# Performance work log

Measured on AMD Instinct MI355X. Metric: run time of the kernel, lower is better.

## Reference

```python
import jax, jax.numpy as jnp
import numpy as np

LMAX = 8
RES_BETA = 32   # Gauss-Legendre points in beta (>= 2*LMAX+1 -> exact quadrature for product)
RES_ALPHA = 63  # uniform points in alpha (>= 2*(2*LMAX)+1)
BATCH = 16384
DIM = (LMAX + 1) ** 2  # 81 real SH coefficients, flat index i = l*l + l + m


def _normalized_assoc_legendre(lmax, y):
    # P[b, l, m] = orthonormalized associated Legendre \bar{P}_l^m(y), 0<=m<=l,
    # normalized so that int_{-1}^{1} Pbar_l^m Pbar_l'^m dy = delta_{ll'} / (2*pi).
    n = len(y)
    P = np.zeros((n, lmax + 1, lmax + 1))
    sx = np.sqrt(np.clip(1.0 - y * y, 0.0, None))
    P[:, 0, 0] = np.sqrt(1.0 / (4.0 * np.pi))
    for m in range(1, lmax + 1):
        P[:, m, m] = -np.sqrt((2.0 * m + 1.0) / (2.0 * m)) * sx * P[:, m - 1, m - 1]
    for m in range(lmax):
        P[:, m + 1, m] = np.sqrt(2.0 * m + 3.0) * y * P[:, m, m]
    for m in range(lmax + 1):
        for l in range(m + 2, lmax + 1):
            a = np.sqrt((4.0 * l * l - 1.0) / (l * l - m * m))
            b = np.sqrt(((l - 1.0) ** 2 - m * m) / (4.0 * (l - 1.0) ** 2 - 1.0))
            P[:, l, m] = a * (y * P[:, l - 1, m] - b * P[:, l - 2, m])
    return P


def _s2grid_basis():
    # Gauss-Legendre nodes y=cos(beta) and weights (integrate sin(beta) d(beta) exactly)
    y, w = np.polynomial.legendre.leggauss(RES_BETA)
    P = _normalized_assoc_legendre(LMAX, y)
    alphas = 2.0 * np.pi * np.arange(RES_ALPHA) / RES_ALPHA
    shb = np.zeros((RES_BETA, DIM))   # Legendre part, per flat (l,m) index
    sha = np.zeros((RES_ALPHA, DIM))  # Fourier part, per flat (l,m) index
    s2 = np.sqrt(2.0)
    for l in range(LMAX + 1):
        for m in range(-l, l + 1):
            i = l * l + l + m
            shb[:, i] = P[:, l, abs(m)]
            if m == 0:
                sha[:, i] = 1.0
            elif m > 0:
                sha[:, i] = s2 * np.cos(m * alphas)
            else:
                sha[:, i] = s2 * np.sin(-m * alphas)
    qw = w * (2.0 * np.pi / RES_ALPHA)  # combined beta quadrature + alpha trapezoid weight
    return (shb.astype(np.float32), sha.astype(np.float32), qw.astype(np.float32))


def setup_inputs() -> dict:
    key = jax.random.key(0)
    k1, k2 = jax.random.split(key)
    shb, sha, qw = _s2grid_basis()
    return {
        "input1": jax.random.normal(k1, (BATCH, DIM), dtype=jnp.float32),
        "input2": jax.random.normal(k2, (BATCH, DIM), dtype=jnp.float32),
        "shb": jnp.asarray(shb),
        "sha": jnp.asarray(sha),
        "qw": jnp.asarray(qw),
    }


def _to_s2grid(x, shb, sha):
    # x: [Z, D] -> grid: [Z, res_beta, res_alpha]
    t = jnp.einsum('zi,bi->zbi', x, shb)        # Legendre expansion along beta
    return jnp.einsum('zbi,ai->zba', t, sha)    # Fourier synthesis along alpha


def _from_s2grid(g, shb, sha, qw):
    # g: [Z, res_beta, res_alpha] -> coeffs: [Z, D]
    t = jnp.einsum('zba,ai->zbi', g, sha)       # Fourier analysis along alpha
    return jnp.einsum('zbi,bi,b->zi', t, shb, qw)  # Legendre projection with quadrature


def reference(input1, input2, shb, sha, qw):
    g1 = _to_s2grid(input1, shb, sha)
    g2 = _to_s2grid(input2, shb, sha)
    return _from_s2grid(g1 * g2, shb, sha, qw)
```

## Files before the change

### kernel.cpp

```cpp
#include <hip/hip_runtime.h>

#define DIM 81
#define RA  63
#define RB  32
#define ZT  32
#define XS  104
#define OS  100

#define OFF_SHAA 0
#define OFF_SHAT 12288
#define OFF_SHBH 24576
#define OFF_SHBQ 30720
#define WS_NEED  43008

typedef _Float16 half8 __attribute__((ext_vector_type(8)));
typedef __fp16  fp16x2 __attribute__((ext_vector_type(2)));
typedef float floatx16 __attribute__((ext_vector_type(16)));

union H8U { unsigned u[4]; half8 h; };
union H2U { fp16x2 h; unsigned u; };

__global__ __launch_bounds__(256) void precompute_fact(
    const float* __restrict__ shb, const float* __restrict__ sha,
    const float* __restrict__ qw, char* __restrict__ wsp)
{
    _Float16* shaAP = (_Float16*)(wsp + OFF_SHAA);
    _Float16* shaTP = (_Float16*)(wsp + OFF_SHAT);
    _Float16* shbHP = (_Float16*)(wsp + OFF_SHBH);
    float*    shbqP = (float*)(wsp + OFF_SHBQ);

    int idx = blockIdx.x * 256 + threadIdx.x;
    if (idx < 6144) {
        int j = idx & 7, lane = (idx >> 3) & 63, g = idx >> 9;
        int at = g / 6, kk = g - at * 6;
        int a = at * 32 + (lane & 31);
        int i = kk * 16 + (lane >> 5) * 8 + j;
        float v = (a < RA && i < DIM) ? sha[a * DIM + i] : 0.f;
        shaAP[idx] = (_Float16)v;
    } else if (idx < 12288) {
        int t = idx - 6144;
        int j = t & 7, lane = (t >> 3) & 63, g = t >> 9;
        int it = g >> 2, ks = g & 3;
        int a = ks * 16 + (lane >> 5) * 8 + j;
        int i = it * 32 + (lane & 31);
        float v = (a < RA && i < DIM) ? sha[a * DIM + i] : 0.f;
        shaTP[t] = (_Float16)v;
    } else if (idx < 15360) {
        int t = idx - 12288;
        int j = t & 7, hi = (t >> 3) & 1, g = t >> 4;
        int b = g / 6, kk = g - b * 6;
        int i = kk * 16 + hi * 8 + j;
        float v = (i < DIM) ? shb[b * DIM + i] : 0.f;
        shbHP[t] = (_Float16)v;
    } else if (idx < 18432) {
        int t = idx - 15360;
        int l = t & 31, g = t >> 5;
        int b = g / 3, it = g - b * 3;
        int i = it * 32 + l;
        float v = (i < DIM) ? shb[b * DIM + i] * qw[b] : 0.f;
        shbqP[t] = v;
    }
}

__global__ __launch_bounds__(256, 1) void gaunt_fact(
    const float* __restrict__ x1, const float* __restrict__ x2,
    const char* __restrict__ wsp, float* __restrict__ out)
{
    const _Float16* shaAP = (const _Float16*)(wsp + OFF_SHAA);
    const _Float16* shaTP = (const _Float16*)(wsp + OFF_SHAT);
    const _Float16* shbHP = (const _Float16*)(wsp + OFF_SHBH);
    const float*    shbqP = (const float*)(wsp + OFF_SHBQ);

    __shared__ __align__(16) char lds[2 * ZT * OS * 4];
    _Float16* xp = (_Float16*)lds;
    float*    ob = (float*)lds;

    const int tid = threadIdx.x;
    const int z0  = blockIdx.x * ZT;

    #pragma unroll
    for (int in = 0; in < 2; ++in) {
        const float* src = in ? x2 : x1;
        _Float16* dst = xp + in * (ZT * XS);
        for (int idx = tid; idx < ZT * 96; idx += 256) {
            int r = idx / 96, c = idx - r * 96;
            float v = (c < DIM) ? src[(size_t)(z0 + r) * DIM + c] : 0.f;
            dst[r * XS + c] = (_Float16)v;
        }
    }
    __syncthreads();

    const int l = tid & 63, l31 = l & 31, hi = l >> 5;
    const int nw = tid >> 6;

    half8 xfr[2][6];
    #pragma unroll
    for (int in = 0; in < 2; ++in)
        #pragma unroll
        for (int kk = 0; kk < 6; ++kk)
            xfr[in][kk] = *(const half8*)(xp + in * (ZT * XS) + l31 * XS + kk * 16 + hi * 8);
    __syncthreads();

    half8 aAc[2][6];
    #pragma unroll
    for (int at = 0; at < 2; ++at)
        #pragma unroll
        for (int kk = 0; kk < 6; ++kk)
            aAc[at][kk] = *(const half8*)(shaAP + ((at * 6 + kk) * 64 + l) * 8);

    floatx16 accO[3];
    #pragma unroll
    for (int it = 0; it < 3; ++it)
        #pragma unroll
        for (int r = 0; r < 16; ++r) accO[it][r] = 0.f;

    #pragma unroll 1
    for (int bi = 0; bi < 8; ++bi) {
        const int b = nw * 8 + bi;

        const float s0 = shbqP[(b * 3 + 0) * 32 + l31];
        const float s1 = shbqP[(b * 3 + 1) * 32 + l31];
        const float s2 = shbqP[(b * 3 + 2) * 32 + l31];

        unsigned f[2][8];
        #pragma unroll
        for (int at = 0; at < 2; ++at) {
            floatx16 g0, g1;
            #pragma unroll
            for (int r = 0; r < 16; ++r) { g0[r] = 0.f; g1[r] = 0.f; }
            #pragma unroll
            for (int kk = 0; kk < 6; ++kk) {
                const half8 sf = *(const half8*)(shbHP + ((b * 6 + kk) * 2 + hi) * 8);
                const half8 aS = aAc[at][kk] * sf;
                g0 = __builtin_amdgcn_mfma_f32_32x32x16_f16(aS, xfr[0][kk], g0, 0, 0, 0);
                g1 = __builtin_amdgcn_mfma_f32_32x32x16_f16(aS, xfr[1][kk], g1, 0, 0, 0);
            }
            unsigned q[8];
            #pragma unroll
            for (int j = 0; j < 8; ++j) {
                H2U t;
                t.h = __builtin_amdgcn_cvt_pkrtz(g0[2 * j] * g1[2 * j], g0[2 * j + 1] * g1[2 * j + 1]);
                q[j] = t.u;
            }
            asm volatile("v_permlane32_swap_b32 %0, %1" : "+v"(q[0]), "+v"(q[2]));
            asm volatile("v_permlane32_swap_b32 %0, %1" : "+v"(q[1]), "+v"(q[3]));
            asm volatile("v_permlane32_swap_b32 %0, %1" : "+v"(q[4]), "+v"(q[6]));
            asm volatile("v_permlane32_swap_b32 %0, %1" : "+v"(q[5]), "+v"(q[7]));
            #pragma unroll
            for (int w = 0; w < 8; ++w) f[at][w] = q[w];
        }

        #pragma unroll
        for (int it = 0; it < 3; ++it) {
            floatx16 R;
            #pragma unroll
            for (int r = 0; r < 16; ++r) R[r] = 0.f;
            #pragma unroll
            for (int at = 0; at < 2; ++at) {
                H8U a0, a1;
                a0.u[0] = f[at][0]; a0.u[1] = f[at][1]; a0.u[2] = f[at][2]; a0.u[3] = f[at][3];
                a1.u[0] = f[at][4]; a1.u[1] = f[at][5]; a1.u[2] = f[at][6]; a1.u[3] = f[at][7];
                half8 bT0 = *(const half8*)(shaTP + ((it * 4 + at * 2) * 64 + l) * 8);
                half8 bT1 = *(const half8*)(shaTP + ((it * 4 + at * 2 + 1) * 64 + l) * 8);
                R = __builtin_amdgcn_mfma_f32_32x32x16_f16(a0.h, bT0, R, 0, 0, 0);
                R = __builtin_amdgcn_mfma_f32_32x32x16_f16(a1.h, bT1, R, 0, 0, 0);
            }
            const float s = (it == 0) ? s0 : (it == 1) ? s1 : s2;
            accO[it] += R * s;
        }
    }

    if (nw >= 2) {
        float* buf = ob + (nw - 2) * (ZT * OS);
        #pragma unroll
        for (int it = 0; it < 3; ++it)
            #pragma unroll
            for (int r = 0; r < 16; ++r)
                buf[((r & 3) + 8 * (r >> 2) + 4 * hi) * OS + it * 32 + l31] = accO[it][r];
    }
    __syncthreads();
    if (nw < 2) {
        float* buf = ob + nw * (ZT * OS);
        #pragma unroll
        for (int it = 0; it < 3; ++it)
            #pragma unroll
            for (int r = 0; r < 16; ++r)
                accO[it][r] += buf[((r & 3) + 8 * (r >> 2) + 4 * hi) * OS + it * 32 + l31];
    }
    __syncthreads();
    if (nw < 2) {
        float* buf = ob + nw * (ZT * OS);
        #pragma unroll
        for (int it = 0; it < 3; ++it)
            #pragma unroll
            for (int r = 0; r < 16; ++r)
                buf[((r & 3) + 8 * (r >> 2) + 4 * hi) * OS + it * 32 + l31] = accO[it][r];
    }
    __syncthreads();

    for (int idx = tid; idx < ZT * DIM; idx += 256) {
        int zz = idx / DIM, ii = idx - zz * DIM;
        out[(size_t)z0 * DIM + idx] = ob[zz * OS + ii] + ob[ZT * OS + zz * OS + ii];
    }
}

__device__ __forceinline__ float wave_sum64(float v) {
    v += __int_as_float(__builtin_amdgcn_update_dpp(0, __float_as_int(v), 0x111, 0xf, 0xf, true));
    v += __int_as_float(__builtin_amdgcn_update_dpp(0, __float_as_int(v), 0x112, 0xf, 0xf, true));
    v += __int_as_float(__builtin_amdgcn_update_dpp(0, __float_as_int(v), 0x114, 0xf, 0xf, true));
    v += __int_as_float(__builtin_amdgcn_update_dpp(0, __float_as_int(v), 0x118, 0xf, 0xf, true));
    v += __int_as_float(__builtin_amdgcn_update_dpp(0, __float_as_int(v), 0x142, 0xf, 0xf, true));
    v += __int_as_float(__builtin_amdgcn_update_dpp(0, __float_as_int(v), 0x143, 0xf, 0xf, true));
    return v;
}

__global__ __launch_bounds__(256) void gaunt_s2grid_kernel(
    const float* __restrict__ x1, const float* __restrict__ x2,
    const float* __restrict__ shb, const float* __restrict__ sha,
    const float* __restrict__ qw, float* __restrict__ out)
{
    __shared__ float sha_s[64 * DIM];
    __shared__ float part[4 * DIM];
    const int tid = threadIdx.x;
    const int z = blockIdx.x;
    for (int idx = tid; idx < 64 * DIM; idx += 256)
        sha_s[idx] = (idx < RA * DIM) ? sha[idx] : 0.0f;
    __syncthreads();
    const int lane = tid & 63;
    const int w = __builtin_amdgcn_readfirstlane(tid >> 6);
    const int b0 = w * 8;
    const float* xz1 = x1 + (size_t)z * DIM;
    const float* xz2 = x2 + (size_t)z * DIM;
    const float* sha_row = sha_s + lane * DIM;
    float g1[8], g2[8];
    #pragma unroll
    for (int bb = 0; bb < 8; ++bb) { g1[bb] = 0.0f; g2[bb] = 0.0f; }
    #pragma unroll 4
    for (int i = 0; i < DIM; ++i) {
        const float sv = sha_row[i];
        const float t1 = xz1[i] * sv, t2 = xz2[i] * sv;
        #pragma unroll
        for (int bb = 0; bb < 8; ++bb) {
            const float h = shb[(b0 + bb) * DIM + i];
            g1[bb] = fmaf(h, t1, g1[bb]);
            g2[bb] = fmaf(h, t2, g2[bb]);
        }
    }
    float q[8];
    #pragma unroll
    for (int bb = 0; bb < 8; ++bb) q[bb] = g1[bb] * g2[bb] * qw[b0 + bb];
    #pragma unroll 4
    for (int i = 0; i < DIM; ++i) {
        float t = 0.0f;
        #pragma unroll
        for (int bb = 0; bb < 8; ++bb) t = fmaf(q[bb], shb[(b0 + bb) * DIM + i], t);
        float v = wave_sum64(t * sha_row[i]);
        if (lane == 63) part[w * DIM + i] = v;
    }
    __syncthreads();
    for (int i = tid; i < DIM; i += 256)
        out[(size_t)z * DIM + i] = part[i] + part[DIM + i] + part[2 * DIM + i] + part[3 * DIM + i];
}

extern "C" void kernel_launch(void* const* d_in, const int* in_sizes, int n_in,
                              void* d_out, int out_size, void* d_ws, size_t ws_size,
                              hipStream_t stream) {
    const float* x1  = (const float*)d_in[0];
    const float* x2  = (const float*)d_in[1];
    const float* shb = (const float*)d_in[2];
    const float* sha = (const float*)d_in[3];
    const float* qw  = (const float*)d_in[4];
    float* out = (float*)d_out;

    const int Z = in_sizes[0] / DIM;

    if (ws_size >= WS_NEED && (Z % ZT) == 0) {
        char* wsp = (char*)d_ws;
        precompute_fact<<<72, 256, 0, stream>>>(shb, sha, qw, wsp);
        gaunt_fact<<<Z / ZT, 256, 0, stream>>>(x1, x2, wsp, out);
    } else {
        gaunt_s2grid_kernel<<<Z, 256, 0, stream>>>(x1, x2, shb, sha, qw, out);
    }
}
```

Before: 42.83 us.

## Stage basis tables in LDS and software-pipeline the per-beta GEMM stages

Each block now copies the precomputed fp16/fp32 basis tables (about 43 KB) from global memory into shared memory and reads them from there instead of from global memory inside the loop. The beta loop is software-pipelined: the grid product for the next beta is computed before the analysis GEMM for the current one, so the two stages' MFMA and permlane work can interleave. The cost is more LDS per block (about 68 KB), which may limit co-resident blocks, a table copy in every block, and higher register pressure from holding two fragment sets.

```diff
diff --git a/kernel.cpp b/kernel.cpp
--- a/kernel.cpp
+++ b/kernel.cpp
@@ -11,7 +11,10 @@
 #define OFF_SHAT 12288
 #define OFF_SHBH 24576
 #define OFF_SHBQ 30720
-#define WS_NEED  43008
+#define TBL_BYTES 43008
+#define WS_NEED   43008
+#define L_XOB     43008
+#define LDS_BYTES (43008 + 25600)
 
 typedef _Float16 half8 __attribute__((ext_vector_type(8)));
 typedef __fp16  fp16x2 __attribute__((ext_vector_type(2)));
@@ -66,17 +69,20 @@
     const float* __restrict__ x1, const float* __restrict__ x2,
     const char* __restrict__ wsp, float* __restrict__ out)
 {
-    const _Float16* shaAP = (const _Float16*)(wsp + OFF_SHAA);
-    const _Float16* shaTP = (const _Float16*)(wsp + OFF_SHAT);
-    const _Float16* shbHP = (const _Float16*)(wsp + OFF_SHBH);
-    const float*    shbqP = (const float*)(wsp + OFF_SHBQ);
-
-    __shared__ __align__(16) char lds[2 * ZT * OS * 4];
-    _Float16* xp = (_Float16*)lds;
-    float*    ob = (float*)lds;
+    __shared__ __align__(16) char lds[LDS_BYTES];
+
+    const _Float16* shaA = (const _Float16*)(lds + OFF_SHAA);
+    const _Float16* shaT = (const _Float16*)(lds + OFF_SHAT);
+    const _Float16* shbH = (const _Float16*)(lds + OFF_SHBH);
+    const float*    shbq = (const float*)(lds + OFF_SHBQ);
+    _Float16* xp = (_Float16*)(lds + L_XOB);
+    float*    ob = (float*)(lds + L_XOB);
 
     const int tid = threadIdx.x;
     const int z0  = blockIdx.x * ZT;
+
+    for (int i = tid; i < TBL_BYTES / 16; i += 256)
+        ((uint4*)lds)[i] = ((const uint4*)wsp)[i];
 
     #pragma unroll
     for (int in = 0; in < 2; ++in) {
@@ -99,14 +105,14 @@
         #pragma unroll
         for (int kk = 0; kk < 6; ++kk)
             xfr[in][kk] = *(const half8*)(xp + in * (ZT * XS) + l31 * XS + kk * 16 + hi * 8);
-    __syncthreads();
 
     half8 aAc[2][6];
     #pragma unroll
     for (int at = 0; at < 2; ++at)
         #pragma unroll
         for (int kk = 0; kk < 6; ++kk)
-            aAc[at][kk] = *(const half8*)(shaAP + ((at * 6 + kk) * 64 + l) * 8);
+            aAc[at][kk] = *(const half8*)(shaA + ((at * 6 + kk) * 64 + l) * 8);
+    __syncthreads();
 
     floatx16 accO[3];
     #pragma unroll
@@ -114,15 +120,7 @@
         #pragma unroll
         for (int r = 0; r < 16; ++r) accO[it][r] = 0.f;
 
-    #pragma unroll 1
-    for (int bi = 0; bi < 8; ++bi) {
-        const int b = nw * 8 + bi;
-
-        const float s0 = shbqP[(b * 3 + 0) * 32 + l31];
-        const float s1 = shbqP[(b * 3 + 1) * 32 + l31];
-        const float s2 = shbqP[(b * 3 + 2) * 32 + l31];
-
-        unsigned f[2][8];
+    auto compute_f = [&](int b, unsigned fO[2][8]) {
         #pragma unroll
         for (int at = 0; at < 2; ++at) {
             floatx16 g0, g1;
@@ -130,7 +128,7 @@
             for (int r = 0; r < 16; ++r) { g0[r] = 0.f; g1[r] = 0.f; }
             #pragma unroll
             for (int kk = 0; kk < 6; ++kk) {
-                const half8 sf = *(const half8*)(shbHP + ((b * 6 + kk) * 2 + hi) * 8);
+                const half8 sf = *(const half8*)(shbH + ((b * 6 + kk) * 2 + hi) * 8);
                 const half8 aS = aAc[at][kk] * sf;
                 g0 = __builtin_amdgcn_mfma_f32_32x32x16_f16(aS, xfr[0][kk], g0, 0, 0, 0);
                 g1 = __builtin_amdgcn_mfma_f32_32x32x16_f16(aS, xfr[1][kk], g1, 0, 0, 0);
@@ -147,9 +145,14 @@
             asm volatile("v_permlane32_swap_b32 %0, %1" : "+v"(q[4]), "+v"(q[6]));
             asm volatile("v_permlane32_swap_b32 %0, %1" : "+v"(q[5]), "+v"(q[7]));
             #pragma unroll
-            for (int w = 0; w < 8; ++w) f[at][w] = q[w];
+            for (int w = 0; w < 8; ++w) fO[at][w] = q[w];
         }
-
+    };
+
+    auto gemm2_acc = [&](int b, const unsigned fI[2][8]) {
+        const float s0 = shbq[(b * 3 + 0) * 32 + l31];
+        const float s1 = shbq[(b * 3 + 1) * 32 + l31];
+        const float s2 = shbq[(b * 3 + 2) * 32 + l31];
         #pragma unroll
         for (int it = 0; it < 3; ++it) {
             floatx16 R;
@@ -158,17 +161,30 @@
             #pragma unroll
             for (int at = 0; at < 2; ++at) {
                 H8U a0, a1;
-                a0.u[0] = f[at][0]; a0.u[1] = f[at][1]; a0.u[2] = f[at][2]; a0.u[3] = f[at][3];
-                a1.u[0] = f[at][4]; a1.u[1] = f[at][5]; a1.u[2] = f[at][6]; a1.u[3] = f[at][7];
-                half8 bT0 = *(const half8*)(shaTP + ((it * 4 + at * 2) * 64 + l) * 8);
-                half8 bT1 = *(const half8*)(shaTP + ((it * 4 + at * 2 + 1) * 64 + l) * 8);
+                a0.u[0] = fI[at][0]; a0.u[1] = fI[at][1]; a0.u[2] = fI[at][2]; a0.u[3] = fI[at][3];
+                a1.u[0] = fI[at][4]; a1.u[1] = fI[at][5]; a1.u[2] = fI[at][6]; a1.u[3] = fI[at][7];
+                half8 bT0 = *(const half8*)(shaT + ((it * 4 + at * 2) * 64 + l) * 8);
+                half8 bT1 = *(const half8*)(shaT + ((it * 4 + at * 2 + 1) * 64 + l) * 8);
                 R = __builtin_amdgcn_mfma_f32_32x32x16_f16(a0.h, bT0, R, 0, 0, 0);
                 R = __builtin_amdgcn_mfma_f32_32x32x16_f16(a1.h, bT1, R, 0, 0, 0);
             }
             const float s = (it == 0) ? s0 : (it == 1) ? s1 : s2;
             accO[it] += R * s;
         }
-    }
+    };
+
+    unsigned fc[2][8], fn[2][8];
+    compute_f(nw * 8, fc);
+    #pragma unroll 1
+    for (int bi = 0; bi < 7; ++bi) {
+        compute_f(nw * 8 + bi + 1, fn);
+        gemm2_acc(nw * 8 + bi, fc);
+        #pragma unroll
+        for (int at = 0; at < 2; ++at)
+            #pragma unroll
+            for (int w = 0; w < 8; ++w) fc[at][w] = fn[at][w];
+    }
+    gemm2_acc(nw * 8 + 7, fc);
 
     if (nw >= 2) {
         float* buf = ob + (nw - 2) * (ZT * OS);
```

Measured after the change: 45.89 us. 1.07x slower.

## Software-pipeline beta loop, hoist shaT fragments to registers, vectorize input load

Applied to the files above, without the earlier changes.

The beta loop is software-pipelined so the forward GEMM and product for the next beta row are issued before the analysis GEMM of the current row, letting independent MFMA chains interleave. The shaT B-fragments are now loaded once into registers instead of being reloaded every iteration. The input staging uses float4 loads and packed half4 stores in place of scalar element copies. This adds register pressure from the extra f buffer and 12 cached half8 fragments, which could cause spills at one wave per SIMD.

```diff
diff --git a/kernel.cpp b/kernel.cpp
--- a/kernel.cpp
+++ b/kernel.cpp
@@ -14,6 +14,7 @@
 #define WS_NEED  43008
 
 typedef _Float16 half8 __attribute__((ext_vector_type(8)));
+typedef _Float16 half4v __attribute__((ext_vector_type(4)));
 typedef __fp16  fp16x2 __attribute__((ext_vector_type(2)));
 typedef float floatx16 __attribute__((ext_vector_type(16)));
 
@@ -78,14 +79,22 @@
     const int tid = threadIdx.x;
     const int z0  = blockIdx.x * ZT;
 
-    #pragma unroll
-    for (int in = 0; in < 2; ++in) {
-        const float* src = in ? x2 : x1;
-        _Float16* dst = xp + in * (ZT * XS);
-        for (int idx = tid; idx < ZT * 96; idx += 256) {
-            int r = idx / 96, c = idx - r * 96;
-            float v = (c < DIM) ? src[(size_t)(z0 + r) * DIM + c] : 0.f;
-            dst[r * XS + c] = (_Float16)v;
+    {
+        const int nv = ZT * 24;
+        #pragma unroll
+        for (int in = 0; in < 2; ++in) {
+            const float* src = in ? x2 : x1;
+            _Float16* dst = xp + in * (ZT * XS);
+            for (int idx = tid; idx < nv; idx += 256) {
+                int r = idx / 24, c4 = idx - r * 24;
+                float4 v = make_float4(0.f, 0.f, 0.f, 0.f);
+                if (c4 < 20)      v = *(const float4*)(src + (size_t)(z0 + r) * DIM + c4 * 4);
+                else if (c4 == 20) v.x = src[(size_t)(z0 + r) * DIM + 80];
+                half4v h;
+                h[0] = (_Float16)v.x; h[1] = (_Float16)v.y;
+                h[2] = (_Float16)v.z; h[3] = (_Float16)v.w;
+                *(half4v*)(dst + r * XS + c4 * 4) = h;
+            }
         }
     }
     __syncthreads();
@@ -108,21 +117,22 @@
         for (int kk = 0; kk < 6; ++kk)
             aAc[at][kk] = *(const half8*)(shaAP + ((at * 6 + kk) * 64 + l) * 8);
 
+    half8 bTc[3][2][2];
+    #pragma unroll
+    for (int it = 0; it < 3; ++it)
+        #pragma unroll
+        for (int at = 0; at < 2; ++at) {
+            bTc[it][at][0] = *(const half8*)(shaTP + ((it * 4 + at * 2) * 64 + l) * 8);
+            bTc[it][at][1] = *(const half8*)(shaTP + ((it * 4 + at * 2 + 1) * 64 + l) * 8);
+        }
+
     floatx16 accO[3];
     #pragma unroll
     for (int it = 0; it < 3; ++it)
         #pragma unroll
         for (int r = 0; r < 16; ++r) accO[it][r] = 0.f;
 
-    #pragma unroll 1
-    for (int bi = 0; bi < 8; ++bi) {
-        const int b = nw * 8 + bi;
-
-        const float s0 = shbqP[(b * 3 + 0) * 32 + l31];
-        const float s1 = shbqP[(b * 3 + 1) * 32 + l31];
-        const float s2 = shbqP[(b * 3 + 2) * 32 + l31];
-
-        unsigned f[2][8];
+    auto compute_f = [&](int b, unsigned fO[2][8]) {
         #pragma unroll
         for (int at = 0; at < 2; ++at) {
             floatx16 g0, g1;
@@ -147,9 +157,14 @@
             asm volatile("v_permlane32_swap_b32 %0, %1" : "+v"(q[4]), "+v"(q[6]));
             asm volatile("v_permlane32_swap_b32 %0, %1" : "+v"(q[5]), "+v"(q[7]));
             #pragma unroll
-            for (int w = 0; w < 8; ++w) f[at][w] = q[w];
-        }
-
+            for (int w = 0; w < 8; ++w) fO[at][w] = q[w];
+        }
+    };
+
+    auto gemm2_acc = [&](int b, const unsigned fI[2][8]) {
+        const float s0 = shbqP[(b * 3 + 0) * 32 + l31];
+        const float s1 = shbqP[(b * 3 + 1) * 32 + l31];
+        const float s2 = shbqP[(b * 3 + 2) * 32 + l31];
         #pragma unroll
         for (int it = 0; it < 3; ++it) {
             floatx16 R;
@@ -158,17 +173,28 @@
             #pragma unroll
             for (int at = 0; at < 2; ++at) {
                 H8U a0, a1;
-                a0.u[0] = f[at][0]; a0.u[1] = f[at][1]; a0.u[2] = f[at][2]; a0.u[3] = f[at][3];
-                a1.u[0] = f[at][4]; a1.u[1] = f[at][5]; a1.u[2] = f[at][6]; a1.u[3] = f[at][7];
-                half8 bT0 = *(const half8*)(shaTP + ((it * 4 + at * 2) * 64 + l) * 8);
-                half8 bT1 = *(const half8*)(shaTP + ((it * 4 + at * 2 + 1) * 64 + l) * 8);
-                R = __builtin_amdgcn_mfma_f32_32x32x16_f16(a0.h, bT0, R, 0, 0, 0);
-                R = __builtin_amdgcn_mfma_f32_32x32x16_f16(a1.h, bT1, R, 0, 0, 0);
+                a0.u[0] = fI[at][0]; a0.u[1] = fI[at][1]; a0.u[2] = fI[at][2]; a0.u[3] = fI[at][3];
+                a1.u[0] = fI[at][4]; a1.u[1] = fI[at][5]; a1.u[2] = fI[at][6]; a1.u[3] = fI[at][7];
+                R = __builtin_amdgcn_mfma_f32_32x32x16_f16(a0.h, bTc[it][at][0], R, 0, 0, 0);
+                R = __builtin_amdgcn_mfma_f32_32x32x16_f16(a1.h, bTc[it][at][1], R, 0, 0, 0);
             }
             const float s = (it == 0) ? s0 : (it == 1) ? s1 : s2;
             accO[it] += R * s;
         }
-    }
+    };
+
+    unsigned fc[2][8], fn[2][8];
+    compute_f(nw * 8, fc);
+    #pragma unroll 1
+    for (int bi = 0; bi < 7; ++bi) {
+        compute_f(nw * 8 + bi + 1, fn);
+        gemm2_acc(nw * 8 + bi, fc);
+        #pragma unroll
+        for (int at = 0; at < 2; ++at)
+            #pragma unroll
+            for (int w = 0; w < 8; ++w) fc[at][w] = fn[at][w];
+    }
+    gemm2_acc(nw * 8 + 7, fc);
 
     if (nw >= 2) {
         float* buf = ob + (nw - 2) * (ZT * OS);
```

Measured after the change: 42.38 us. No clear change (-1.0%).

## Exploit parity symmetry of Gauss-Legendre nodes to halve forward grid GEMMs

Applied to the files above, without the earlier changes.

Coefficients are permuted so even-parity (l+|m|) terms come first and odd-parity terms last. For each beta node b, one pass of even and odd partial sums yields the grid for both b and its mirror 31-b: the sum gives b and the difference gives the mirror. This halves the synthesis MFMA work. The shb tables are also staged in LDS, and sha A-fragments are loaded per iteration instead of held in registers. The cost is an extra gather through a permutation table during input load and more live accumulators per pass.

```diff
diff --git a/kernel.cpp b/kernel.cpp
--- a/kernel.cpp
+++ b/kernel.cpp
@@ -11,7 +11,11 @@
 #define OFF_SHAT 12288
 #define OFF_SHBH 24576
 #define OFF_SHBQ 30720
-#define WS_NEED  43008
+#define OFF_PERM 43008
+#define WS_NEED  43392
+
+#define LDS_TBL   18432
+#define LDS_BYTES (18432 + 25600)
 
 typedef _Float16 half8 __attribute__((ext_vector_type(8)));
 typedef __fp16  fp16x2 __attribute__((ext_vector_type(2)));
@@ -19,6 +23,20 @@
 
 union H8U { unsigned u[4]; half8 h; };
 union H2U { fp16x2 h; unsigned u; };
+
+__device__ int src_of_k(int k) {
+    const int want = (k < 48) ? 0 : 1;
+    const int rank = (k < 48) ? k : k - 48;
+    int cnt = 0;
+    for (int i = 0; i < DIM; ++i) {
+        int l = 0;
+        while ((l + 1) * (l + 1) <= i) ++l;
+        int m = i - l * l - l;
+        int p = (l + (m < 0 ? -m : m)) & 1;
+        if (p == want) { if (cnt == rank) return i; ++cnt; }
+    }
+    return -1;
+}
 
 __global__ __launch_bounds__(256) void precompute_fact(
     const float* __restrict__ shb, const float* __restrict__ sha,
@@ -28,14 +46,16 @@
     _Float16* shaTP = (_Float16*)(wsp + OFF_SHAT);
     _Float16* shbHP = (_Float16*)(wsp + OFF_SHBH);
     float*    shbqP = (float*)(wsp + OFF_SHBQ);
+    int*      permP = (int*)(wsp + OFF_PERM);
 
     int idx = blockIdx.x * 256 + threadIdx.x;
     if (idx < 6144) {
         int j = idx & 7, lane = (idx >> 3) & 63, g = idx >> 9;
         int at = g / 6, kk = g - at * 6;
         int a = at * 32 + (lane & 31);
-        int i = kk * 16 + (lane >> 5) * 8 + j;
-        float v = (a < RA && i < DIM) ? sha[a * DIM + i] : 0.f;
+        int k = kk * 16 + (lane >> 5) * 8 + j;
+        int si = src_of_k(k);
+        float v = (a < RA && si >= 0) ? sha[a * DIM + si] : 0.f;
         shaAP[idx] = (_Float16)v;
     } else if (idx < 12288) {
         int t = idx - 6144;
@@ -49,8 +69,9 @@
         int t = idx - 12288;
         int j = t & 7, hi = (t >> 3) & 1, g = t >> 4;
         int b = g / 6, kk = g - b * 6;
-        int i = kk * 16 + hi * 8 + j;
-        float v = (i < DIM) ? shb[b * DIM + i] : 0.f;
+        int k = kk * 16 + hi * 8 + j;
+        int si = src_of_k(k);
+        float v = (si >= 0) ? shb[b * DIM + si] : 0.f;
         shbHP[t] = (_Float16)v;
     } else if (idx < 18432) {
         int t = idx - 15360;
@@ -59,8 +80,49 @@
         int i = it * 32 + l;
         float v = (i < DIM) ? shb[b * DIM + i] * qw[b] : 0.f;
         shbqP[t] = v;
-    }
-}
+    } else if (idx < 18528) {
+        permP[idx - 18432] = src_of_k(idx - 18432);
+    }
+}
+
+#define G1_PAIR(AT, FB, FP) do {                                                            \
+    floatx16 e0, e1, o0, o1;                                                                \
+    _Pragma("unroll") for (int r = 0; r < 16; ++r) { e0[r]=0.f; e1[r]=0.f; o0[r]=0.f; o1[r]=0.f; } \
+    _Pragma("unroll") for (int kk = 0; kk < 3; ++kk) {                                      \
+        const half8 sf = *(const half8*)(shbH_l + ((b * 6 + kk) * 2 + hi) * 8);             \
+        const half8 aA = *(const half8*)(shaAP + (((AT) * 6 + kk) * 64 + l) * 8);           \
+        const half8 aS = aA * sf;                                                           \
+        e0 = __builtin_amdgcn_mfma_f32_32x32x16_f16(aS, xfr[0][kk], e0, 0, 0, 0);           \
+        e1 = __builtin_amdgcn_mfma_f32_32x32x16_f16(aS, xfr[1][kk], e1, 0, 0, 0);           \
+    }                                                                                       \
+    _Pragma("unroll") for (int kk = 3; kk < 6; ++kk) {                                      \
+        const half8 sf = *(const half8*)(shbH_l + ((b * 6 + kk) * 2 + hi) * 8);             \
+        const half8 aA = *(const half8*)(shaAP + (((AT) * 6 + kk) * 64 + l) * 8);           \
+        const half8 aS = aA * sf;                                                           \
+        o0 = __builtin_amdgcn_mfma_f32_32x32x16_f16(aS, xfr[0][kk], o0, 0, 0, 0);           \
+        o1 = __builtin_amdgcn_mfma_f32_32x32x16_f16(aS, xfr[1][kk], o1, 0, 0, 0);           \
+    }                                                                                       \
+    unsigned qb[8], qm[8];                                                                  \
+    _Pragma("unroll") for (int j = 0; j < 8; ++j) {                                         \
+        H2U tb, tm;                                                                         \
+        float pb0 = (e0[2*j]   + o0[2*j])   * (e1[2*j]   + o1[2*j]);                        \
+        float pb1 = (e0[2*j+1] + o0[2*j+1]) * (e1[2*j+1] + o1[2*j+1]);                      \
+        tb.h = __builtin_amdgcn_cvt_pkrtz(pb0, pb1);                                        \
+        float pm0 = (e0[2*j]   - o0[2*j])   * (e1[2*j]   - o1[2*j]);                        \
+        float pm1 = (e0[2*j+1] - o0[2*j+1]) * (e1[2*j+1] - o1[2*j+1]);                      \
+        tm.h = __builtin_amdgcn_cvt_pkrtz(pm0, pm1);                                        \
+        qb[j] = tb.u; qm[j] = tm.u;                                                         \
+    }                                                                                       \
+    asm volatile("v_permlane32_swap_b32 %0, %1" : "+v"(qb[0]), "+v"(qb[2]));                \
+    asm volatile("v_permlane32_swap_b32 %0, %1" : "+v"(qb[1]), "+v"(qb[3]));                \
+    asm volatile("v_permlane32_swap_b32 %0, %1" : "+v"(qb[4]), "+v"(qb[6]));                \
+    asm volatile("v_permlane32_swap_b32 %0, %1" : "+v"(qb[5]), "+v"(qb[7]));                \
+    asm volatile("v_permlane32_swap_b32 %0, %1" : "+v"(qm[0]), "+v"(qm[2]));                \
+    asm volatile("v_permlane32_swap_b32 %0, %1" : "+v"(qm[1]), "+v"(qm[3]));                \
+    asm volatile("v_permlane32_swap_b32 %0, %1" : "+v"(qm[4]), "+v"(qm[6]));                \
+    asm volatile("v_permlane32_swap_b32 %0, %1" : "+v"(qm[5]), "+v"(qm[7]));                \
+    _Pragma("unroll") for (int w = 0; w < 8; ++w) { FB[w] = qb[w]; FP[w] = qm[w]; }         \
+} while (0)
 
 __global__ __launch_bounds__(256, 1) void gaunt_fact(
     const float* __restrict__ x1, const float* __restrict__ x2,
@@ -68,25 +130,27 @@
 {
     const _Float16* shaAP = (const _Float16*)(wsp + OFF_SHAA);
     const _Float16* shaTP = (const _Float16*)(wsp + OFF_SHAT);
-    const _Float16* shbHP = (const _Float16*)(wsp + OFF_SHBH);
-    const float*    shbqP = (const float*)(wsp + OFF_SHBQ);
-
-    __shared__ __align__(16) char lds[2 * ZT * OS * 4];
-    _Float16* xp = (_Float16*)lds;
-    float*    ob = (float*)lds;
+    const int*      permG = (const int*)(wsp + OFF_PERM);
+
+    __shared__ __align__(16) char lds[LDS_BYTES];
+    const _Float16* shbH_l = (const _Float16*)lds;
+    const float*    shbq_l = (const float*)(lds + 6144);
+    _Float16* xp = (_Float16*)(lds + LDS_TBL);
+    float*    ob = (float*)(lds + LDS_TBL);
 
     const int tid = threadIdx.x;
     const int z0  = blockIdx.x * ZT;
 
-    #pragma unroll
-    for (int in = 0; in < 2; ++in) {
+    for (int i = tid; i < LDS_TBL / 16; i += 256)
+        ((uint4*)lds)[i] = ((const uint4*)(wsp + OFF_SHBH))[i];
+
+    for (int idx = tid; idx < 2 * ZT * 96; idx += 256) {
+        int in = idx / (ZT * 96), t = idx - in * (ZT * 96);
+        int r = t / 96, c = t - r * 96;
+        int si = permG[c];
         const float* src = in ? x2 : x1;
-        _Float16* dst = xp + in * (ZT * XS);
-        for (int idx = tid; idx < ZT * 96; idx += 256) {
-            int r = idx / 96, c = idx - r * 96;
-            float v = (c < DIM) ? src[(size_t)(z0 + r) * DIM + c] : 0.f;
-            dst[r * XS + c] = (_Float16)v;
-        }
+        float v = (si >= 0) ? src[(size_t)(z0 + r) * DIM + si] : 0.f;
+        xp[in * (ZT * XS) + r * XS + c] = (_Float16)v;
     }
     __syncthreads();
 
@@ -101,73 +165,55 @@
             xfr[in][kk] = *(const half8*)(xp + in * (ZT * XS) + l31 * XS + kk * 16 + hi * 8);
     __syncthreads();
 
-    half8 aAc[2][6];
-    #pragma unroll
-    for (int at = 0; at < 2; ++at)
-        #pragma unroll
-        for (int kk = 0; kk < 6; ++kk)
-            aAc[at][kk] = *(const half8*)(shaAP + ((at * 6 + kk) * 64 + l) * 8);
-
     floatx16 accO[3];
     #pragma unroll
     for (int it = 0; it < 3; ++it)
         #pragma unroll
         for (int r = 0; r < 16; ++r) accO[it][r] = 0.f;
 
-    #pragma unroll 1
-    for (int bi = 0; bi < 8; ++bi) {
-        const int b = nw * 8 + bi;
-
-        const float s0 = shbqP[(b * 3 + 0) * 32 + l31];
-        const float s1 = shbqP[(b * 3 + 1) * 32 + l31];
-        const float s2 = shbqP[(b * 3 + 2) * 32 + l31];
-
-        unsigned f[2][8];
-        #pragma unroll
-        for (int at = 0; at < 2; ++at) {
-            floatx16 g0, g1;
-            #pragma unroll
-            for (int r = 0; r < 16; ++r) { g0[r] = 0.f; g1[r] = 0.f; }
-            #pragma unroll
-            for (int kk = 0; kk < 6; ++kk) {
-                const half8 sf = *(const half8*)(shbHP + ((b * 6 + kk) * 2 + hi) * 8);
-                const half8 aS = aAc[at][kk] * sf;
-                g0 = __builtin_amdgcn_mfma_f32_32x32x16_f16(aS, xfr[0][kk], g0, 0, 0, 0);
-                g1 = __builtin_amdgcn_mfma_f32_32x32x16_f16(aS, xfr[1][kk], g1, 0, 0, 0);
-            }
-            unsigned q[8];
-            #pragma unroll
-            for (int j = 0; j < 8; ++j) {
-                H2U t;
-                t.h = __builtin_amdgcn_cvt_pkrtz(g0[2 * j] * g1[2 * j], g0[2 * j + 1] * g1[2 * j + 1]);
-                q[j] = t.u;
-            }
-            asm volatile("v_permlane32_swap_b32 %0, %1" : "+v"(q[0]), "+v"(q[2]));
-            asm volatile("v_permlane32_swap_b32 %0, %1" : "+v"(q[1]), "+v"(q[3]));
-            asm volatile("v_permlane32_swap_b32 %0, %1" : "+v"(q[4]), "+v"(q[6]));
-            asm volatile("v_permlane32_swap_b32 %0, %1" : "+v"(q[5]), "+v"(q[7]));
-            #pragma unroll
-            for (int w = 0; w < 8; ++w) f[at][w] = q[w];
-        }
-
+    auto gemm2_acc = [&](int bb, const unsigned* fa0, const unsigned* fa1) {
+        const float s0 = shbq_l[(bb * 3 + 0) * 32 + l31];
+        const float s1 = shbq_l[(bb * 3 + 1) * 32 + l31];
+        const float s2 = shbq_l[(bb * 3 + 2) * 32 + l31];
         #pragma unroll
         for (int it = 0; it < 3; ++it) {
             floatx16 R;
             #pragma unroll
             for (int r = 0; r < 16; ++r) R[r] = 0.f;
-            #pragma unroll
-            for (int at = 0; at < 2; ++at) {
+            {
+                const half8 bT0 = *(const half8*)(shaTP + ((it * 4 + 0) * 64 + l) * 8);
+                const half8 bT1 = *(const half8*)(shaTP + ((it * 4 + 1) * 64 + l) * 8);
                 H8U a0, a1;
-                a0.u[0] = f[at][0]; a0.u[1] = f[at][1]; a0.u[2] = f[at][2]; a0.u[3] = f[at][3];
-                a1.u[0] = f[at][4]; a1.u[1] = f[at][5]; a1.u[2] = f[at][6]; a1.u[3] = f[at][7];
-                half8 bT0 = *(const half8*)(shaTP + ((it * 4 + at * 2) * 64 + l) * 8);
-                half8 bT1 = *(const half8*)(shaTP + ((it * 4 + at * 2 + 1) * 64 + l) * 8);
+                a0.u[0] = fa0[0]; a0.u[1] = fa0[1]; a0.u[2] = fa0[2]; a0.u[3] = fa0[3];
+                a1.u[0] = fa0[4]; a1.u[1] = fa0[5]; a1.u[2] = fa0[6]; a1.u[3] = fa0[7];
+                R = __builtin_amdgcn_mfma_f32_32x32x16_f16(a0.h, bT0, R, 0, 0, 0);
+                R = __builtin_amdgcn_mfma_f32_32x32x16_f16(a1.h, bT1, R, 0, 0, 0);
+            }
+            {
+                const half8 bT0 = *(const half8*)(shaTP + ((it * 4 + 2) * 64 + l) * 8);
+                const half8 bT1 = *(const half8*)(shaTP + ((it * 4 + 3) * 64 + l) * 8);
+                H8U a0, a1;
+                a0.u[0] = fa1[0]; a0.u[1] = fa1[1]; a0.u[2] = fa1[2]; a0.u[3] = fa1[3];
+                a1.u[0] = fa1[4]; a1.u[1] = fa1[5]; a1.u[2] = fa1[6]; a1.u[3] = fa1[7];
                 R = __builtin_amdgcn_mfma_f32_32x32x16_f16(a0.h, bT0, R, 0, 0, 0);
                 R = __builtin_amdgcn_mfma_f32_32x32x16_f16(a1.h, bT1, R, 0, 0, 0);
             }
             const float s = (it == 0) ? s0 : (it == 1) ? s1 : s2;
             accO[it] += R * s;
         }
+    };
+
+    #pragma unroll 1
+    for (int pi = 0; pi < 4; ++pi) {
+        const int b  = nw * 4 + pi;
+        const int bp = 31 - b;
+
+        unsigned fB0[8], fB1[8], fP0[8], fP1[8];
+        G1_PAIR(0, fB0, fP0);
+        G1_PAIR(1, fB1, fP1);
+
+        gemm2_acc(b,  fB0, fB1);
+        gemm2_acc(bp, fP0, fP1);
     }
 
     if (nw >= 2) {
@@ -276,7 +322,7 @@
 
     if (ws_size >= WS_NEED && (Z % ZT) == 0) {
         char* wsp = (char*)d_ws;
-        precompute_fact<<<72, 256, 0, stream>>>(shb, sha, qw, wsp);
+        precompute_fact<<<73, 256, 0, stream>>>(shb, sha, qw, wsp);
         gaunt_fact<<<Z / ZT, 256, 0, stream>>>(x1, x2, wsp, out);
     } else {
         gaunt_s2grid_kernel<<<Z, 256, 0, stream>>>(x1, x2, shb, sha, qw, out);
```

Result: slower. 58.19 us (+35.9%).
